# Optimization experiments

Measured on AMD Instinct MI355X. Metric: run time of the kernel, lower is better.

Reference implementation:

```python
import jax, jax.numpy as jnp
import numpy as np
import math

H = 16
D_ATTN = 64
D_MID = 64
D_X = 1024
D_Z = 1024
D_OUT = 1024
B = 2
L_X = 2048
L_Z = 2048
MINUS_INFINITY = -1000000.0

def _xavier(key, shape):
    fan_in, fan_out = shape
    limit = math.sqrt(6.0 / (fan_in + fan_out))
    return jax.random.uniform(key, shape, jnp.float32, -limit, limit)

def setup_inputs() -> dict:
    key = jax.random.key(0)
    ks = jax.random.split(key, 8)
    primary = jax.random.normal(ks[0], (B, L_X, D_X), jnp.float32)
    context = jax.random.normal(ks[1], (B, L_Z, D_Z), jnp.float32)
    padding_mask = jnp.ones((B, L_Z), jnp.int32)
    # causal attention mask (b, l_x, l_z)
    attention_mask = jnp.broadcast_to(
        jnp.tril(jnp.ones((L_X, L_Z), jnp.int32))[None], (B, L_X, L_Z))
    W_qs = _xavier(ks[2], (D_X, H * D_ATTN))
    W_ks = _xavier(ks[3], (D_Z, H * D_ATTN))
    W_vs = _xavier(ks[4], (D_Z, H * D_MID))
    W_o = _xavier(ks[5], (H * D_MID, D_OUT))
    b_o = jnp.zeros((D_OUT,), jnp.float32)
    return {"primary": primary, "context": context,
            "padding_mask": padding_mask, "attention_mask": attention_mask,
            "W_qs": W_qs, "W_ks": W_ks, "W_vs": W_vs, "W_o": W_o, "b_o": b_o}

def reference(primary, context, padding_mask, attention_mask, W_qs, W_ks, W_vs, W_o, b_o):
    b, l_x, _ = primary.shape
    l_z = context.shape[1]
    # QKV projections, split into heads (head-major columns)
    q = (primary @ W_qs).reshape(b, l_x, H, D_ATTN).transpose(0, 2, 1, 3)  # (b,h,l_x,d_attn)
    k = (context @ W_ks).reshape(b, l_z, H, D_ATTN).transpose(0, 2, 1, 3)  # (b,h,l_z,d_attn)
    v = (context @ W_vs).reshape(b, l_z, H, D_MID).transpose(0, 2, 1, 3)   # (b,h,l_z,d_mid)
    scores = jnp.einsum('bhxd,bhzd->bhxz', q, k) / math.sqrt(D_ATTN)
    # combined mask: attention_mask AND padding_mask, broadcast over heads
    mask = (attention_mask * padding_mask[:, None, :])[:, None]  # (b,1,l_x,l_z)
    scores = jnp.where(mask == 0, MINUS_INFINITY, scores)
    attn = jax.nn.softmax(scores, axis=-1)
    out = jnp.einsum('bhxz,bhzm->bhxm', attn, v)  # (b,h,l_x,d_mid)
    out = out.transpose(0, 2, 1, 3).reshape(b, l_x, H * D_MID)
    return out @ W_o + b_o
```

## Files before the change

kernel.cpp:

```cpp
#include <hip/hip_runtime.h>

#define NB 2
#define LX 2048
#define LZ 2048
#define HH 16
#define DA 64
#define DM 64
#define HD 1024
#define KVS 2048
#define MINF  -1000000.0f
#define QSC   0.1803368801f
#define DTHR  8.0f

typedef __attribute__((ext_vector_type(8))) short short8;
typedef __attribute__((ext_vector_type(4))) float f32x4;

static __device__ __forceinline__ ushort f2bf(float f) {
    union { float f; uint32_t u; } c; c.f = f;
    return (ushort)((c.u + 0x7FFFu + ((c.u >> 16) & 1u)) >> 16);
}

static __device__ __forceinline__ float bf2f(ushort u) {
    union { uint32_t u; float f; } c; c.u = (uint32_t)u << 16;
    return c.f;
}

static __device__ __forceinline__ uint32_t cvtpk(float lo, float hi) {
    uint32_t r;
    asm("v_cvt_pk_bf16_f32 %0, %1, %2" : "=v"(r) : "v"(lo), "v"(hi));
    return r;
}

#define GL16(g, l) __builtin_amdgcn_global_load_lds( \
    (const __attribute__((address_space(1))) void*)(g), \
    (__attribute__((address_space(3))) void*)(l), 16, 0, 0)

__global__ __launch_bounds__(256) void prep(
    const float* __restrict__ pA, const float* __restrict__ pB,
    ushort* __restrict__ oA, ushort* __restrict__ oB,
    const float* __restrict__ W0, const float* __restrict__ W1,
    const float* __restrict__ W2, const float* __restrict__ W3,
    ushort* __restrict__ T0, ushort* __restrict__ T1,
    ushort* __restrict__ T2, ushort* __restrict__ T3,
    const int* __restrict__ amask, const int* __restrict__ pmask,
    int* __restrict__ cls)
{
    const int fid = blockIdx.x;
    const int t = threadIdx.x;
    if (fid < 8192) {
        const int i = fid * 256 + t;
        const float* in = (i < 1048576) ? pA : pB;
        ushort* out = (i < 1048576) ? oA : oB;
        const int j = i & 1048575;
        float4 v = ((const float4*)in)[j];
        ushort4 o;
        o.x = f2bf(v.x); o.y = f2bf(v.y); o.z = f2bf(v.z); o.w = f2bf(v.w);
        ((ushort4*)out)[j] = o;
    } else if (fid < 9216) {
        __shared__ ushort Ls[64][72];
        const int id2 = fid - 8192;
        const int zz = id2 >> 8, rem = id2 & 255;
        const float* W = (zz == 0) ? W0 : (zz == 1) ? W1 : (zz == 2) ? W2 : W3;
        ushort* Wt = (zz == 0) ? T0 : (zz == 1) ? T1 : (zz == 2) ? T2 : T3;
        const int n0 = (rem & 15) * 64, k0 = (rem >> 4) * 64;
        const int rr = t >> 4, c4 = (t & 15) * 4;
        #pragma unroll
        for (int i = 0; i < 4; ++i) {
            const int r = rr + i * 16;
            float4 v = *(const float4*)&W[(size_t)(k0 + r) * 1024 + n0 + c4];
            Ls[c4 + 0][r] = f2bf(v.x);
            Ls[c4 + 1][r] = f2bf(v.y);
            Ls[c4 + 2][r] = f2bf(v.z);
            Ls[c4 + 3][r] = f2bf(v.w);
        }
        __syncthreads();
        const int n = t >> 2, kc = (t & 3) * 16;
        *(short8*)&Wt[(size_t)(n0 + n) * 1024 + k0 + kc]     = *(const short8*)&Ls[n][kc];
        *(short8*)&Wt[(size_t)(n0 + n) * 1024 + k0 + kc + 8] = *(const short8*)&Ls[n][kc + 8];
    } else {
        const int bid = fid - 9216;
        const int b = bid >> 10, xb = (bid >> 5) & 31, zb = bid & 31;
        int andv = 1, orv = 0;
        #pragma unroll
        for (int i = 0; i < 16; ++i) {
            const int e = t + i * 256;
            const int r = e >> 6, z = e & 63;
            const int m = amask[((size_t)b * LX + xb * 64 + r) * LZ + zb * 64 + z];
            const int p = pmask[(size_t)b * LZ + zb * 64 + z];
            const int v = (m != 0) & (p != 0);
            andv &= v; orv |= v;
        }
        __shared__ int sa[256];
        __shared__ int so[256];
        sa[t] = andv; so[t] = orv;
        __syncthreads();
        for (int s = 128; s > 0; s >>= 1) {
            if (t < s) { sa[t] &= sa[t + s]; so[t] |= so[t + s]; }
            __syncthreads();
        }
        if (t == 0) cls[bid] = so[0] ? (sa[0] ? 1 : 2) : 0;
    }
}

__global__ __launch_bounds__(256) void gemm_qkv(
    const ushort* __restrict__ Pb, const ushort* __restrict__ Cb,
    const ushort* __restrict__ Wqt, const ushort* __restrict__ Wkvt,
    ushort* __restrict__ Qb, ushort* __restrict__ KV)
{
    const int bx = blockIdx.x;
    const bool isQ = bx < 8;
    const ushort* A  = isQ ? Pb : Cb;
    const ushort* Bt = isQ ? Wqt : Wkvt;
    ushort* Cout = isQ ? Qb : KV;
    const int n0 = (isQ ? bx : bx - 8) * 128;
    const int ostr = isQ ? 1024 : KVS;
    const float osc = isQ ? QSC : 1.0f;

    __shared__ ushort As[128 * 32];
    __shared__ ushort Bs[128 * 32];
    const int t = threadIdx.x;
    const int w = t >> 6, l = t & 63, lr = l & 15, lg = l >> 4;
    const int wr = w >> 1, wc = w & 1;
    const int m0 = blockIdx.y * 128;

    const int c0 = t, c1 = t + 256;
    const ushort* a0 = &A[(size_t)(m0 + (c0 >> 2)) * 1024 + (c0 & 3) * 8];
    const ushort* a1 = &A[(size_t)(m0 + (c1 >> 2)) * 1024 + (c1 & 3) * 8];
    const ushort* b0 = &Bt[(size_t)(n0 + (c0 >> 2)) * 1024 + (c0 & 3) * 8];
    const ushort* b1 = &Bt[(size_t)(n0 + (c1 >> 2)) * 1024 + (c1 & 3) * 8];
    ushort* lA0 = &As[w * 512];
    ushort* lA1 = &As[(4 + w) * 512];
    ushort* lB0 = &Bs[w * 512];
    ushort* lB1 = &Bs[(4 + w) * 512];

    f32x4 acc[4][4];
    #pragma unroll
    for (int i = 0; i < 4; ++i)
        #pragma unroll
        for (int j = 0; j < 4; ++j) acc[i][j] = 0.f;

    for (int k0 = 0; k0 < 1024; k0 += 32) {
        __syncthreads();
        GL16(a0 + k0, lA0);
        GL16(a1 + k0, lA1);
        GL16(b0 + k0, lB0);
        GL16(b1 + k0, lB1);
        __syncthreads();
        short8 af[4], bf[4];
        #pragma unroll
        for (int mi = 0; mi < 4; ++mi)
            af[mi] = *(const short8*)&As[(wr * 64 + mi * 16 + lr) * 32 + lg * 8];
        #pragma unroll
        for (int nj = 0; nj < 4; ++nj)
            bf[nj] = *(const short8*)&Bs[(wc * 64 + nj * 16 + lr) * 32 + lg * 8];
        #pragma unroll
        for (int mi = 0; mi < 4; ++mi)
            #pragma unroll
            for (int nj = 0; nj < 4; ++nj)
                acc[mi][nj] = __builtin_amdgcn_mfma_f32_16x16x32_bf16(
                    af[mi], bf[nj], acc[mi][nj], 0, 0, 0);
    }

    const int row0 = m0 + wr * 64, col0 = n0 + wc * 64;
    #pragma unroll
    for (int mi = 0; mi < 4; ++mi)
        #pragma unroll
        for (int nj = 0; nj < 4; ++nj) {
            const int col = col0 + nj * 16 + lr;
            #pragma unroll
            for (int r = 0; r < 4; ++r) {
                const int row = row0 + mi * 16 + lg * 4 + r;
                Cout[(size_t)row * ostr + col] = f2bf(acc[mi][nj][r] * osc);
            }
        }
}

__global__ __launch_bounds__(256, 4) void attn_mfma(
    const ushort* __restrict__ Qg, const ushort* __restrict__ KVg,
    const int* __restrict__ amask, const int* __restrict__ pmask,
    const int* __restrict__ cls, ushort* __restrict__ Op,
    float2* __restrict__ ml)
{
    __shared__ ushort Ks[64 * 72];
    __shared__ ushort Vt[64 * 64];

    const int t = threadIdx.x, w = t >> 6, l = t & 63, lr = l & 15, lg = l >> 4;
    const int flat = blockIdx.x + 32 * (blockIdx.y + 16 * blockIdx.z);
    const int xcd = flat & 7, ii = flat >> 3;
    const int g = xcd + 8 * (ii >> 5);
    const int xr_ = ii & 31;
    const int h = g & 15, bs = g >> 4;
    const int b = bs & 1, sKV = bs >> 1;
    const int fx = (xr_ & 1) ? 31 - (xr_ >> 1) : (xr_ >> 1);
    const int qb = b ? 31 - fx : fx;
    const int qw = qb * 64 + w * 16;

    short8 qf[2];
    #pragma unroll
    for (int ks = 0; ks < 2; ++ks)
        qf[ks] = *(const short8*)&Qg[(size_t)(b * LX + qw + lr) * HD
                                     + h * DA + ks * 32 + lg * 8];

    float mrun = -1e30f, lrun = 0.f;
    f32x4 o[4];
    #pragma unroll
    for (int mj = 0; mj < 4; ++mj) o[mj] = 0.f;

    const int kz = t >> 2, kc = (t & 3) * 16;
    const int vz = (t >> 3) * 2, vc = (t & 7) * 8;

    for (int zb = sKV; zb < LZ / 64; zb += 2) {
        const int cl = cls[b * 1024 + qb * 32 + zb];
        if (cl == 0) continue;
        const int z0 = zb * 64;

        __syncthreads();
        {
            const ushort* kp = &KVg[(size_t)(b * LZ + z0 + kz) * KVS + h * DA + kc];
            *(short8*)&Ks[kz * 72 + kc]     = *(const short8*)kp;
            *(short8*)&Ks[kz * 72 + kc + 8] = *(const short8*)(kp + 8);
            const ushort* vp = &KVg[(size_t)(b * LZ + z0 + vz) * KVS + 1024 + h * DM + vc];
            short8 v0 = *(const short8*)vp;
            short8 v1 = *(const short8*)(vp + KVS);
            const int zc = vz >> 3, zo = vz & 7;
            #pragma unroll
            for (int j = 0; j < 8; ++j) {
                const int m = vc + j;
                const int idx = m * 64 + (((zc ^ m ^ (m >> 3)) & 7) << 3) + zo;
                *(uint32_t*)&Vt[idx] =
                    (uint32_t)(ushort)v0[j] | ((uint32_t)(ushort)v1[j] << 16);
            }
        }
        __syncthreads();

        f32x4 s[4];
        __builtin_amdgcn_s_setprio(1);
        #pragma unroll
        for (int nj = 0; nj < 4; ++nj) {
            const short8 kf0 = *(const short8*)&Ks[(nj * 16 + lr) * 72 + lg * 8];
            const short8 kf1 = *(const short8*)&Ks[(nj * 16 + lr) * 72 + 32 + lg * 8];
            f32x4 z4 = 0.f;
            z4 = __builtin_amdgcn_mfma_f32_16x16x32_bf16(kf0, qf[0], z4, 0, 0, 0);
            z4 = __builtin_amdgcn_mfma_f32_16x16x32_bf16(kf1, qf[1], z4, 0, 0, 0);
            s[nj] = z4;
        }
        __builtin_amdgcn_s_setprio(0);
        if (cl == 2) {
            const size_t arow = (size_t)(b * LX + qw + lr) * LZ + z0;
            #pragma unroll
            for (int nj = 0; nj < 4; ++nj)
                #pragma unroll
                for (int r = 0; r < 4; ++r) {
                    const int z = nj * 16 + lg * 4 + r;
                    const int ok = (amask[arow + z] != 0) & (pmask[b * LZ + z0 + z] != 0);
                    if (!ok) s[nj][r] = MINF;
                }
        }
        {
            float pm = s[0][0];
            #pragma unroll
            for (int nj = 0; nj < 4; ++nj)
                #pragma unroll
                for (int r = 0; r < 4; ++r) pm = fmaxf(pm, s[nj][r]);
            pm = fmaxf(pm, __shfl_xor(pm, 16));
            pm = fmaxf(pm, __shfl_xor(pm, 32));
            if (__any(pm > mrun + DTHR)) {
                const float mn = fmaxf(mrun, pm);
                const float al = exp2f(mrun - mn);
                mrun = mn;
                lrun *= al;
                #pragma unroll
                for (int r = 0; r < 4; ++r) {
                    const float alq = __shfl(al, (lg << 2) + r);
                    #pragma unroll
                    for (int mj = 0; mj < 4; ++mj) o[mj][r] *= alq;
                }
            }
            #pragma unroll
            for (int nj = 0; nj < 4; ++nj)
                #pragma unroll
                for (int r = 0; r < 4; ++r) {
                    const float p = exp2f(s[nj][r] - mrun);
                    s[nj][r] = p;
                    lrun += p;
                }
        }
        short8 pa[2];
        {
            uint32_t pk01[4], pk23[4];
            #pragma unroll
            for (int nj = 0; nj < 4; ++nj) {
                pk01[nj] = cvtpk(s[nj][0], s[nj][1]);
                pk23[nj] = cvtpk(s[nj][2], s[nj][3]);
            }
            #pragma unroll
            for (int ks = 0; ks < 2; ++ks) {
                union { uint32_t d[4]; short8 v; } u;
                u.d[0] = pk01[2 * ks];
                u.d[1] = pk23[2 * ks];
                u.d[2] = pk01[2 * ks + 1];
                u.d[3] = pk23[2 * ks + 1];
                pa[ks] = u.v;
            }
        }
        __builtin_amdgcn_s_setprio(1);
        #pragma unroll
        for (int mj = 0; mj < 4; ++mj) {
            const int m_ = mj * 16 + lr;
            const int xr = (m_ ^ (m_ >> 3)) & 7;
            const int czb = lg >> 1;
            const int zo = (lg & 1) * 4;
            #pragma unroll
            for (int ks = 0; ks < 2; ++ks) {
                const int clo = (ks * 4 + czb) ^ xr;
                const int chi = (ks * 4 + 2 + czb) ^ xr;
                const uint2 lo = *(const uint2*)&Vt[m_ * 64 + ((clo & 7) << 3) + zo];
                const uint2 hi = *(const uint2*)&Vt[m_ * 64 + ((chi & 7) << 3) + zo];
                union { uint32_t d[4]; short8 v; } u;
                u.d[0] = lo.x; u.d[1] = lo.y; u.d[2] = hi.x; u.d[3] = hi.y;
                o[mj] = __builtin_amdgcn_mfma_f32_16x16x32_bf16(pa[ks], u.v, o[mj], 0, 0, 0);
            }
        }
        __builtin_amdgcn_s_setprio(0);
    }

    lrun += __shfl_xor(lrun, 16);
    lrun += __shfl_xor(lrun, 32);
    if (l < 16)
        ml[(size_t)((sKV * NB + b) * HH + h) * LX + qw + l] = make_float2(mrun, lrun);
    const size_t ob = (size_t)((sKV * NB + b) * LX + qw) * HD + h * DM;
    #pragma unroll
    for (int r = 0; r < 4; ++r)
        #pragma unroll
        for (int mj = 0; mj < 4; ++mj)
            Op[ob + (size_t)((lg << 2) + r) * HD + mj * 16 + lr] = f2bf(o[mj][r]);
}

__global__ __launch_bounds__(256) void gemm_out_fused(
    const ushort* __restrict__ Op, const float2* __restrict__ ml,
    const ushort* __restrict__ Bt, const float* __restrict__ bias,
    float* __restrict__ Cout)
{
    __shared__ ushort As[64 * 32];
    __shared__ ushort Bs[128 * 32];
    __shared__ float2 Wl[64][17];
    const int t = threadIdx.x;
    const int w = t >> 6, l = t & 63, lr = l & 15, lg = l >> 4;
    const int wr = w >> 1, wc = w & 1;
    const int n0 = blockIdx.x * 128, m0 = blockIdx.y * 64;

    {
        const int e = t * 4;
        #pragma unroll
        for (int j = 0; j < 4; ++j) {
            const int rl = (e + j) >> 4, hh = (e + j) & 15;
            const int ra = m0 + rl;
            const int bb = ra >> 11, xx = ra & 2047;
            const float2 a0 = ml[(size_t)(bb * HH + hh) * LX + xx];
            const float2 a1 = ml[(size_t)((NB + bb) * HH + hh) * LX + xx];
            const float M = fmaxf(a0.x, a1.x);
            const float w0 = exp2f(a0.x - M), w1 = exp2f(a1.x - M);
            const float inv = 1.f / fmaxf(a0.y * w0 + a1.y * w1, 1e-37f);
            Wl[rl][hh] = make_float2(w0 * inv, w1 * inv);
        }
    }
    __syncthreads();

    const int ra = m0 + (t >> 2), ka = (t & 3) * 8;
    const ushort* p0 = &Op[(size_t)ra * HD + ka];
    const ushort* p1 = p0 + (size_t)NB * LX * HD;
    const ushort* b0 = &Bt[(size_t)(n0 + (t >> 2)) * 1024 + ka];
    const ushort* b1 = &Bt[(size_t)(n0 + 64 + (t >> 2)) * 1024 + ka];
    ushort* lB0 = &Bs[w * 512];
    ushort* lB1 = &Bs[(4 + w) * 512];

    f32x4 acc[2][4];
    #pragma unroll
    for (int i = 0; i < 2; ++i)
        #pragma unroll
        for (int j = 0; j < 4; ++j) acc[i][j] = 0.f;

    for (int k0 = 0; k0 < 1024; k0 += 32) {
        const short8 q0 = *(const short8*)(p0 + k0);
        const short8 q1 = *(const short8*)(p1 + k0);
        const float2 wv = Wl[t >> 2][(k0 + ka) >> 6];
        union { ushort d[8]; short8 v; } av;
        #pragma unroll
        for (int j = 0; j < 8; ++j)
            av.d[j] = f2bf(bf2f((ushort)q0[j]) * wv.x + bf2f((ushort)q1[j]) * wv.y);
        __syncthreads();
        *(short8*)&As[t * 8] = av.v;
        GL16(b0 + k0, lB0);
        GL16(b1 + k0, lB1);
        __syncthreads();
        short8 af[2], bf[4];
        #pragma unroll
        for (int mi = 0; mi < 2; ++mi)
            af[mi] = *(const short8*)&As[(wr * 32 + mi * 16 + lr) * 32 + lg * 8];
        #pragma unroll
        for (int nj = 0; nj < 4; ++nj)
            bf[nj] = *(const short8*)&Bs[(wc * 64 + nj * 16 + lr) * 32 + lg * 8];
        #pragma unroll
        for (int mi = 0; mi < 2; ++mi)
            #pragma unroll
            for (int nj = 0; nj < 4; ++nj)
                acc[mi][nj] = __builtin_amdgcn_mfma_f32_16x16x32_bf16(
                    af[mi], bf[nj], acc[mi][nj], 0, 0, 0);
    }

    const int row0 = m0 + wr * 32, col0 = n0 + wc * 64;
    #pragma unroll
    for (int mi = 0; mi < 2; ++mi)
        #pragma unroll
        for (int nj = 0; nj < 4; ++nj) {
            const int col = col0 + nj * 16 + lr;
            #pragma unroll
            for (int r = 0; r < 4; ++r) {
                const int row = row0 + mi * 16 + lg * 4 + r;
                Cout[(size_t)row * 1024 + col] = acc[mi][nj][r] + bias[col];
            }
        }
}

extern "C" void kernel_launch(void* const* d_in, const int* in_sizes, int n_in,
                              void* d_out, int out_size, void* d_ws, size_t ws_size,
                              hipStream_t stream)
{
    const float* primary = (const float*)d_in[0];
    const float* context = (const float*)d_in[1];
    const int*   pmask   = (const int*)d_in[2];
    const int*   amask   = (const int*)d_in[3];
    const float* Wq      = (const float*)d_in[4];
    const float* Wk      = (const float*)d_in[5];
    const float* Wv      = (const float*)d_in[6];
    const float* Wo      = (const float*)d_in[7];
    const float* bo      = (const float*)d_in[8];
    float* out = (float*)d_out;

    char* w8 = (char*)d_ws;
    ushort* Pb  = (ushort*)(w8 + 0);
    ushort* Cb  = (ushort*)(w8 + 8388608);
    ushort* Qb  = (ushort*)(w8 + 16777216);
    ushort* KV  = (ushort*)(w8 + 25165824);
    ushort* Wqt = (ushort*)(w8 + 50331648);
    ushort* Wkt = (ushort*)(w8 + 52428800);
    ushort* Wvt = (ushort*)(w8 + 54525952);
    ushort* Wot = (ushort*)(w8 + 56623104);
    int*    clsp = (int*)(w8 + 58720256);
    ushort* Op   = Pb;
    float2* mlp  = (float2*)Wqt;

    prep<<<11264, 256, 0, stream>>>(primary, context, Pb, Cb,
                                    Wq, Wk, Wv, Wo, Wqt, Wkt, Wvt, Wot,
                                    amask, pmask, clsp);
    gemm_qkv<<<dim3(24, 32), 256, 0, stream>>>(Pb, Cb, Wqt, Wkt, Qb, KV);
    attn_mfma<<<dim3(32, 16, 4), 256, 0, stream>>>(Qb, KV, amask, pmask, clsp, Op, mlp);
    gemm_out_fused<<<dim3(8, 64), 256, 0, stream>>>(Op, mlp, Wot, bo, out);
}
```

Baseline: 134.9 us.

## Rewrite QKV GEMM with 256x256 tiles and triple-buffered async LDS pipeline

Replaces the 128x128 QKV projection GEMM with a 512-thread kernel computing 256x256 tiles. It uses a three-stage LDS ring buffer, so global-to-LDS loads for stage k+2 are issued while MFMAs run on stage k. It synchronises with vmcnt waits plus a single barrier per step and raises wave priority around the MFMA block. The larger tiles raise arithmetic intensity but cut the grid to 192 blocks, which may underfill the GPU, and the 96KB of LDS limits occupancy.

```diff
diff --git a/kernel.cpp b/kernel.cpp
--- a/kernel.cpp
+++ b/kernel.cpp
@@ -102,68 +102,103 @@
     }
 }
 
-__global__ __launch_bounds__(256) void gemm_qkv(
+__global__ __launch_bounds__(512, 2) void gemm_qkv256(
     const ushort* __restrict__ Pb, const ushort* __restrict__ Cb,
     const ushort* __restrict__ Wqt, const ushort* __restrict__ Wkvt,
     ushort* __restrict__ Qb, ushort* __restrict__ KV)
 {
-    const int bx = blockIdx.x;
-    const bool isQ = bx < 8;
+    __shared__ ushort lds[49152];
+
+    const int bid = blockIdx.x;
+    const bool isQ = bid < 64;
     const ushort* A  = isQ ? Pb : Cb;
     const ushort* Bt = isQ ? Wqt : Wkvt;
     ushort* Cout = isQ ? Qb : KV;
-    const int n0 = (isQ ? bx : bx - 8) * 128;
     const int ostr = isQ ? 1024 : KVS;
     const float osc = isQ ? QSC : 1.0f;
-
-    __shared__ ushort As[128 * 32];
-    __shared__ ushort Bs[128 * 32];
+    int mt, nt;
+    if (isQ) { mt = bid >> 2; nt = bid & 3; }
+    else     { const int i2 = bid - 64; mt = i2 >> 3; nt = i2 & 7; }
+    const int m0 = mt * 256, n0 = nt * 256;
+
     const int t = threadIdx.x;
     const int w = t >> 6, l = t & 63, lr = l & 15, lg = l >> 4;
-    const int wr = w >> 1, wc = w & 1;
-    const int m0 = blockIdx.y * 128;
-
-    const int c0 = t, c1 = t + 256;
-    const ushort* a0 = &A[(size_t)(m0 + (c0 >> 2)) * 1024 + (c0 & 3) * 8];
-    const ushort* a1 = &A[(size_t)(m0 + (c1 >> 2)) * 1024 + (c1 & 3) * 8];
-    const ushort* b0 = &Bt[(size_t)(n0 + (c0 >> 2)) * 1024 + (c0 & 3) * 8];
-    const ushort* b1 = &Bt[(size_t)(n0 + (c1 >> 2)) * 1024 + (c1 & 3) * 8];
-    ushort* lA0 = &As[w * 512];
-    ushort* lA1 = &As[(4 + w) * 512];
-    ushort* lB0 = &Bs[w * 512];
-    ushort* lB1 = &Bs[(4 + w) * 512];
-
-    f32x4 acc[4][4];
-    #pragma unroll
-    for (int i = 0; i < 4; ++i)
-        #pragma unroll
-        for (int j = 0; j < 4; ++j) acc[i][j] = 0.f;
-
-    for (int k0 = 0; k0 < 1024; k0 += 32) {
-        __syncthreads();
-        GL16(a0 + k0, lA0);
-        GL16(a1 + k0, lA1);
-        GL16(b0 + k0, lB0);
-        GL16(b1 + k0, lB1);
-        __syncthreads();
-        short8 af[4], bf[4];
-        #pragma unroll
-        for (int mi = 0; mi < 4; ++mi)
-            af[mi] = *(const short8*)&As[(wr * 64 + mi * 16 + lr) * 32 + lg * 8];
+    const int wm = w >> 2, wn = w & 3;
+
+    const int rA0 = t >> 2, cA0 = (t & 3) * 8;
+    const int rA1 = (t + 512) >> 2, cA1 = ((t + 512) & 3) * 8;
+    const ushort* srcA0 = &A[(size_t)(m0 + rA0) * 1024 + cA0];
+    const ushort* srcA1 = &A[(size_t)(m0 + rA1) * 1024 + cA1];
+    const ushort* srcB0 = &Bt[(size_t)(n0 + rA0) * 1024 + cA0];
+    const ushort* srcB1 = &Bt[(size_t)(n0 + rA1) * 1024 + cA1];
+    const int dA0 = (w * 64) * 8;
+    const int dA1 = (w * 64 + 512) * 8;
+
+    int aoff[8], boff[4];
+    #pragma unroll
+    for (int mi = 0; mi < 8; ++mi) {
+        const int row = wm * 128 + mi * 16 + lr;
+        aoff[mi] = row * 32 + lg * 8;
+    }
+    #pragma unroll
+    for (int nj = 0; nj < 4; ++nj) {
+        const int row = wn * 64 + nj * 16 + lr;
+        boff[nj] = 8192 + row * 32 + lg * 8;
+    }
+
+#define QSTAGE(kk, bufbase) do {                                   \
+        const int k0s = (kk) * 32;                                 \
+        GL16(srcA0 + k0s, &lds[(bufbase) + dA0]);                  \
+        GL16(srcA1 + k0s, &lds[(bufbase) + dA1]);                  \
+        GL16(srcB0 + k0s, &lds[(bufbase) + 8192 + dA0]);           \
+        GL16(srcB1 + k0s, &lds[(bufbase) + 8192 + dA1]);           \
+    } while (0)
+
+    f32x4 acc[8][4];
+    #pragma unroll
+    for (int mi = 0; mi < 8; ++mi)
+        #pragma unroll
+        for (int nj = 0; nj < 4; ++nj) acc[mi][nj] = 0.f;
+
+    int bcur = 0, bnxt = 16384, bnx2 = 32768;
+
+    QSTAGE(0, bcur);
+    QSTAGE(1, bnxt);
+    asm volatile("s_waitcnt vmcnt(4)" ::: "memory");
+    __builtin_amdgcn_s_barrier();
+    __builtin_amdgcn_sched_barrier(0);
+
+    for (int j = 0; j < 32; ++j) {
+        QSTAGE((j + 2) & 31, bnx2);
+
+        short8 af[8], bf[4];
+        #pragma unroll
+        for (int mi = 0; mi < 8; ++mi)
+            af[mi] = *(const short8*)&lds[bcur + aoff[mi]];
         #pragma unroll
         for (int nj = 0; nj < 4; ++nj)
-            bf[nj] = *(const short8*)&Bs[(wc * 64 + nj * 16 + lr) * 32 + lg * 8];
-        #pragma unroll
-        for (int mi = 0; mi < 4; ++mi)
+            bf[nj] = *(const short8*)&lds[bcur + boff[nj]];
+
+        __builtin_amdgcn_s_setprio(1);
+        #pragma unroll
+        for (int mi = 0; mi < 8; ++mi)
             #pragma unroll
             for (int nj = 0; nj < 4; ++nj)
                 acc[mi][nj] = __builtin_amdgcn_mfma_f32_16x16x32_bf16(
                     af[mi], bf[nj], acc[mi][nj], 0, 0, 0);
-    }
-
-    const int row0 = m0 + wr * 64, col0 = n0 + wc * 64;
-    #pragma unroll
-    for (int mi = 0; mi < 4; ++mi)
+        __builtin_amdgcn_s_setprio(0);
+
+        asm volatile("s_waitcnt vmcnt(4)" ::: "memory");
+        __builtin_amdgcn_s_barrier();
+        __builtin_amdgcn_sched_barrier(0);
+
+        const int tmp = bcur; bcur = bnxt; bnxt = bnx2; bnx2 = tmp;
+    }
+#undef QSTAGE
+
+    const int row0 = m0 + wm * 128, col0 = n0 + wn * 64;
+    #pragma unroll
+    for (int mi = 0; mi < 8; ++mi)
         #pragma unroll
         for (int nj = 0; nj < 4; ++nj) {
             const int col = col0 + nj * 16 + lr;
@@ -453,7 +488,7 @@
     prep<<<11264, 256, 0, stream>>>(primary, context, Pb, Cb,
                                     Wq, Wk, Wv, Wo, Wqt, Wkt, Wvt, Wot,
                                     amask, pmask, clsp);
-    gemm_qkv<<<dim3(24, 32), 256, 0, stream>>>(Pb, Cb, Wqt, Wkt, Qb, KV);
+    gemm_qkv256<<<192, 512, 0, stream>>>(Pb, Cb, Wqt, Wkt, Qb, KV);
     attn_mfma<<<dim3(32, 16, 4), 256, 0, stream>>>(Qb, KV, amask, pmask, clsp, Op, mlp);
     gemm_out_fused<<<dim3(8, 64), 256, 0, stream>>>(Op, mlp, Wot, bo, out);
 }
```

After: 135.4 us. About the same (+0.4%).

## Double-buffer K/V tiles in LDS with register prefetch and ballot-based block skipping

Applied to the files above, without the earlier changes.

The attention kernel now double-buffers the K and V^T tiles in shared memory. The next active key block's global loads are issued into registers before computing on the current block, so load latency overlaps the MFMA and softmax work, and only one barrier is needed per iteration. The per-block class lookups are replaced with two wave ballots that build bitmasks of active and mixed blocks, and workgroups with no active blocks write neutral outputs and exit early. This costs double the LDS and extra live registers, which may reduce occupancy under launch_bounds(256,4).

```diff
diff --git a/kernel.cpp b/kernel.cpp
--- a/kernel.cpp
+++ b/kernel.cpp
@@ -181,8 +181,8 @@
     const int* __restrict__ cls, ushort* __restrict__ Op,
     float2* __restrict__ ml)
 {
-    __shared__ ushort Ks[64 * 72];
-    __shared__ ushort Vt[64 * 64];
+    __shared__ ushort Ks[2][64 * 72];
+    __shared__ ushort Vt[2][64 * 64];
 
     const int t = threadIdx.x, w = t >> 6, l = t & 63, lr = l & 15, lg = l >> 4;
     const int flat = blockIdx.x + 32 * (blockIdx.y + 16 * blockIdx.z);
@@ -195,6 +195,24 @@
     const int qb = b ? 31 - fx : fx;
     const int qw = qb * 64 + w * 16;
 
+    const uint32_t halfm = sKV ? 0xAAAAAAAAu : 0x55555555u;
+    const int cv = cls[b * 1024 + qb * 32 + (l & 31)];
+    const uint32_t act = (uint32_t)__ballot(cv != 0) & halfm;
+    const uint32_t mix = (uint32_t)__ballot(cv == 2) & halfm;
+
+    const size_t obase = (size_t)((sKV * NB + b) * LX + qw) * HD + h * DM;
+    if (act == 0) {
+        if (l < 16)
+            ml[(size_t)((sKV * NB + b) * HH + h) * LX + qw + l]
+                = make_float2(-1e30f, 0.f);
+        #pragma unroll
+        for (int r = 0; r < 4; ++r)
+            #pragma unroll
+            for (int mj = 0; mj < 4; ++mj)
+                Op[obase + (size_t)((lg << 2) + r) * HD + mj * 16 + lr] = 0;
+        return;
+    }
+
     short8 qf[2];
     #pragma unroll
     for (int ks = 0; ks < 2; ++ks)
@@ -209,43 +227,61 @@
     const int kz = t >> 2, kc = (t & 3) * 16;
     const int vz = (t >> 3) * 2, vc = (t & 7) * 8;
 
-    for (int zb = sKV; zb < LZ / 64; zb += 2) {
-        const int cl = cls[b * 1024 + qb * 32 + zb];
-        if (cl == 0) continue;
+    short8 kr0, kr1, vr0, vr1;
+
+#define PREFETCH(zbx) do {                                                     \
+        const int z0p = (zbx) * 64;                                           \
+        const ushort* kp = &KVg[(size_t)(b * LZ + z0p + kz) * KVS + h * DA + kc];\
+        kr0 = *(const short8*)kp;                                             \
+        kr1 = *(const short8*)(kp + 8);                                       \
+        const ushort* vp = &KVg[(size_t)(b * LZ + z0p + vz) * KVS + 1024 + h * DM + vc];\
+        vr0 = *(const short8*)vp;                                             \
+        vr1 = *(const short8*)(vp + KVS);                                     \
+    } while (0)
+
+#define WRITE_LDS(bi) do {                                                     \
+        *(short8*)&Ks[bi][kz * 72 + kc]     = kr0;                            \
+        *(short8*)&Ks[bi][kz * 72 + kc + 8] = kr1;                            \
+        const int zc = vz >> 3, zo = vz & 7;                                  \
+        _Pragma("unroll")                                                      \
+        for (int j = 0; j < 8; ++j) {                                         \
+            const int m = vc + j;                                             \
+            const int idx = m * 64 + (((zc ^ m ^ (m >> 3)) & 7) << 3) + zo;   \
+            *(uint32_t*)&Vt[bi][idx] =                                        \
+                (uint32_t)(ushort)vr0[j] | ((uint32_t)(ushort)vr1[j] << 16);  \
+        }                                                                      \
+    } while (0)
+
+    int zb = __builtin_ctz(act);
+    uint32_t rem = act & (act - 1);
+    PREFETCH(zb);
+    WRITE_LDS(0);
+    __syncthreads();
+    int cur = 0;
+
+    for (;;) {
+        const bool mixed = (mix >> zb) & 1;
         const int z0 = zb * 64;
-
-        __syncthreads();
-        {
-            const ushort* kp = &KVg[(size_t)(b * LZ + z0 + kz) * KVS + h * DA + kc];
-            *(short8*)&Ks[kz * 72 + kc]     = *(const short8*)kp;
-            *(short8*)&Ks[kz * 72 + kc + 8] = *(const short8*)(kp + 8);
-            const ushort* vp = &KVg[(size_t)(b * LZ + z0 + vz) * KVS + 1024 + h * DM + vc];
-            short8 v0 = *(const short8*)vp;
-            short8 v1 = *(const short8*)(vp + KVS);
-            const int zc = vz >> 3, zo = vz & 7;
-            #pragma unroll
-            for (int j = 0; j < 8; ++j) {
-                const int m = vc + j;
-                const int idx = m * 64 + (((zc ^ m ^ (m >> 3)) & 7) << 3) + zo;
-                *(uint32_t*)&Vt[idx] =
-                    (uint32_t)(ushort)v0[j] | ((uint32_t)(ushort)v1[j] << 16);
-            }
-        }
-        __syncthreads();
+        int zbn = -1;
+        if (rem) {
+            zbn = __builtin_ctz(rem);
+            rem &= rem - 1;
+            PREFETCH(zbn);
+        }
 
         f32x4 s[4];
         __builtin_amdgcn_s_setprio(1);
         #pragma unroll
         for (int nj = 0; nj < 4; ++nj) {
-            const short8 kf0 = *(const short8*)&Ks[(nj * 16 + lr) * 72 + lg * 8];
-            const short8 kf1 = *(const short8*)&Ks[(nj * 16 + lr) * 72 + 32 + lg * 8];
+            const short8 kf0 = *(const short8*)&Ks[cur][(nj * 16 + lr) * 72 + lg * 8];
+            const short8 kf1 = *(const short8*)&Ks[cur][(nj * 16 + lr) * 72 + 32 + lg * 8];
             f32x4 z4 = 0.f;
             z4 = __builtin_amdgcn_mfma_f32_16x16x32_bf16(kf0, qf[0], z4, 0, 0, 0);
             z4 = __builtin_amdgcn_mfma_f32_16x16x32_bf16(kf1, qf[1], z4, 0, 0, 0);
             s[nj] = z4;
         }
         __builtin_amdgcn_s_setprio(0);
-        if (cl == 2) {
+        if (mixed) {
             const size_t arow = (size_t)(b * LX + qw + lr) * LZ + z0;
             #pragma unroll
             for (int nj = 0; nj < 4; ++nj)
@@ -314,26 +350,33 @@
             for (int ks = 0; ks < 2; ++ks) {
                 const int clo = (ks * 4 + czb) ^ xr;
                 const int chi = (ks * 4 + 2 + czb) ^ xr;
-                const uint2 lo = *(const uint2*)&Vt[m_ * 64 + ((clo & 7) << 3) + zo];
-                const uint2 hi = *(const uint2*)&Vt[m_ * 64 + ((chi & 7) << 3) + zo];
+                const uint2 lo = *(const uint2*)&Vt[cur][m_ * 64 + ((clo & 7) << 3) + zo];
+                const uint2 hi = *(const uint2*)&Vt[cur][m_ * 64 + ((chi & 7) << 3) + zo];
                 union { uint32_t d[4]; short8 v; } u;
                 u.d[0] = lo.x; u.d[1] = lo.y; u.d[2] = hi.x; u.d[3] = hi.y;
                 o[mj] = __builtin_amdgcn_mfma_f32_16x16x32_bf16(pa[ks], u.v, o[mj], 0, 0, 0);
             }
         }
         __builtin_amdgcn_s_setprio(0);
+
+        if (zbn < 0) break;
+        WRITE_LDS(cur ^ 1);
+        __syncthreads();
+        cur ^= 1;
+        zb = zbn;
     }
 
     lrun += __shfl_xor(lrun, 16);
     lrun += __shfl_xor(lrun, 32);
     if (l < 16)
         ml[(size_t)((sKV * NB + b) * HH + h) * LX + qw + l] = make_float2(mrun, lrun);
-    const size_t ob = (size_t)((sKV * NB + b) * LX + qw) * HD + h * DM;
     #pragma unroll
     for (int r = 0; r < 4; ++r)
         #pragma unroll
         for (int mj = 0; mj < 4; ++mj)
-            Op[ob + (size_t)((lg << 2) + r) * HD + mj * 16 + lr] = f2bf(o[mj][r]);
+            Op[obase + (size_t)((lg << 2) + r) * HD + mj * 16 + lr] = f2bf(o[mj][r]);
+#undef PREFETCH
+#undef WRITE_LDS
 }
 
 __global__ __launch_bounds__(256) void gemm_out_fused(
```

New measurement: 137.4 us. No clear change (+1.9%).

## Write V transposed from QKV GEMM and load V fragments directly in attention

Applied to the files above, without the earlier changes.

The QKV GEMM now writes K into its own buffer and V transposed (head-dim major), staging the transpose through shared memory. The attention kernel drops its per-tile LDS V transpose. It loads K with swizzled direct global-to-LDS copies and reads V fragments straight from global memory into registers. Blocks whose KV tiles are all masked now exit early and write zeros. This removes LDS scatter work and one barrier per tile, at the cost of extra epilogue work in the GEMM and uncached global V reads that may add latency.

```diff
diff --git a/kernel.cpp b/kernel.cpp
--- a/kernel.cpp
+++ b/kernel.cpp
@@ -7,7 +7,6 @@
 #define DA 64
 #define DM 64
 #define HD 1024
-#define KVS 2048
 #define MINF  -1000000.0f
 #define QSC   0.1803368801f
 #define DTHR  8.0f
@@ -105,19 +104,20 @@
 __global__ __launch_bounds__(256) void gemm_qkv(
     const ushort* __restrict__ Pb, const ushort* __restrict__ Cb,
     const ushort* __restrict__ Wqt, const ushort* __restrict__ Wkvt,
-    ushort* __restrict__ Qb, ushort* __restrict__ KV)
+    ushort* __restrict__ Qb, ushort* __restrict__ Kb, ushort* __restrict__ VT)
 {
+    __shared__ ushort sh[8704];
+    ushort* As = sh;
+    ushort* Bs = sh + 4096;
+
     const int bx = blockIdx.x;
     const bool isQ = bx < 8;
+    const bool isV = bx >= 16;
     const ushort* A  = isQ ? Pb : Cb;
     const ushort* Bt = isQ ? Wqt : Wkvt;
-    ushort* Cout = isQ ? Qb : KV;
     const int n0 = (isQ ? bx : bx - 8) * 128;
-    const int ostr = isQ ? 1024 : KVS;
     const float osc = isQ ? QSC : 1.0f;
 
-    __shared__ ushort As[128 * 32];
-    __shared__ ushort Bs[128 * 32];
     const int t = threadIdx.x;
     const int w = t >> 6, l = t & 63, lr = l & 15, lg = l >> 4;
     const int wr = w >> 1, wc = w & 1;
@@ -161,28 +161,54 @@
                     af[mi], bf[nj], acc[mi][nj], 0, 0, 0);
     }
 
-    const int row0 = m0 + wr * 64, col0 = n0 + wc * 64;
-    #pragma unroll
-    for (int mi = 0; mi < 4; ++mi)
-        #pragma unroll
-        for (int nj = 0; nj < 4; ++nj) {
-            const int col = col0 + nj * 16 + lr;
-            #pragma unroll
-            for (int r = 0; r < 4; ++r) {
-                const int row = row0 + mi * 16 + lg * 4 + r;
-                Cout[(size_t)row * ostr + col] = f2bf(acc[mi][nj][r] * osc);
-            }
-        }
+    if (!isV) {
+        ushort* Cout = isQ ? Qb : Kb;
+        const int row0 = m0 + wr * 64, col0 = n0 + wc * 64;
+        #pragma unroll
+        for (int mi = 0; mi < 4; ++mi)
+            #pragma unroll
+            for (int nj = 0; nj < 4; ++nj) {
+                const int col = col0 + nj * 16 + lr;
+                #pragma unroll
+                for (int r = 0; r < 4; ++r) {
+                    const int row = row0 + mi * 16 + lg * 4 + r;
+                    Cout[(size_t)row * 1024 + col] = f2bf(acc[mi][nj][r] * osc);
+                }
+            }
+    } else {
+        #pragma unroll
+        for (int h2 = 0; h2 < 2; ++h2) {
+            __syncthreads();
+            if (wc == h2) {
+                #pragma unroll
+                for (int nj = 0; nj < 4; ++nj)
+                    #pragma unroll
+                    for (int mi = 0; mi < 4; ++mi)
+                        #pragma unroll
+                        for (int r = 0; r < 4; ++r)
+                            sh[(nj * 16 + lr) * 136 + wr * 64 + mi * 16 + lg * 4 + r]
+                                = f2bf(acc[mi][nj][r]);
+            }
+            __syncthreads();
+            const int vcl = t >> 2, seg = t & 3;
+            const int vcol = (n0 - 1024) + h2 * 64 + vcl;
+            ushort* dst = &VT[(size_t)vcol * 4096 + m0 + seg * 32];
+            const ushort* srcl = &sh[vcl * 136 + seg * 32];
+            *(short8*)(dst + 0)  = *(const short8*)(srcl + 0);
+            *(short8*)(dst + 8)  = *(const short8*)(srcl + 8);
+            *(short8*)(dst + 16) = *(const short8*)(srcl + 16);
+            *(short8*)(dst + 24) = *(const short8*)(srcl + 24);
+        }
+    }
 }
 
 __global__ __launch_bounds__(256, 4) void attn_mfma(
-    const ushort* __restrict__ Qg, const ushort* __restrict__ KVg,
-    const int* __restrict__ amask, const int* __restrict__ pmask,
-    const int* __restrict__ cls, ushort* __restrict__ Op,
-    float2* __restrict__ ml)
+    const ushort* __restrict__ Qg, const ushort* __restrict__ Kb,
+    const ushort* __restrict__ VT, const int* __restrict__ amask,
+    const int* __restrict__ pmask, const int* __restrict__ cls,
+    ushort* __restrict__ Op, float2* __restrict__ ml)
 {
-    __shared__ ushort Ks[64 * 72];
-    __shared__ ushort Vt[64 * 64];
+    __shared__ ushort Ks[64 * 64];
 
     const int t = threadIdx.x, w = t >> 6, l = t & 63, lr = l & 15, lg = l >> 4;
     const int flat = blockIdx.x + 32 * (blockIdx.y + 16 * blockIdx.z);
@@ -195,6 +221,24 @@
     const int qb = b ? 31 - fx : fx;
     const int qw = qb * 64 + w * 16;
 
+    const uint32_t halfm = sKV ? 0xAAAAAAAAu : 0x55555555u;
+    const int cv = cls[b * 1024 + qb * 32 + (l & 31)];
+    const uint32_t act = (uint32_t)__ballot(cv != 0) & halfm;
+    const uint32_t mix = (uint32_t)__ballot(cv == 2) & halfm;
+
+    const size_t obase = (size_t)((sKV * NB + b) * LX + qw) * HD + h * DM;
+    if (act == 0) {
+        if (l < 16)
+            ml[(size_t)((sKV * NB + b) * HH + h) * LX + qw + l]
+                = make_float2(-1e30f, 0.f);
+        #pragma unroll
+        for (int r = 0; r < 4; ++r)
+            #pragma unroll
+            for (int mj = 0; mj < 4; ++mj)
+                Op[obase + (size_t)((lg << 2) + r) * HD + mj * 16 + lr] = 0;
+        return;
+    }
+
     short8 qf[2];
     #pragma unroll
     for (int ks = 0; ks < 2; ++ks)
@@ -206,8 +250,12 @@
     #pragma unroll
     for (int mj = 0; mj < 4; ++mj) o[mj] = 0.f;
 
-    const int kz = t >> 2, kc = (t & 3) * 16;
-    const int vz = (t >> 3) * 2, vc = (t & 7) * 8;
+    const int zs0 = t >> 3, zs1 = 32 + (t >> 3);
+    const int cs = t & 7;
+    const int gc0 = (cs ^ (zs0 & 7)) << 3;
+    ushort* dst0 = &Ks[w * 512];
+    ushort* dst1 = &Ks[2048 + w * 512];
+    const size_t kbase = (size_t)(b * LZ) * 1024 + h * DA;
 
     for (int zb = sKV; zb < LZ / 64; zb += 2) {
         const int cl = cls[b * 1024 + qb * 32 + zb];
@@ -215,30 +263,29 @@
         const int z0 = zb * 64;
 
         __syncthreads();
-        {
-            const ushort* kp = &KVg[(size_t)(b * LZ + z0 + kz) * KVS + h * DA + kc];
-            *(short8*)&Ks[kz * 72 + kc]     = *(const short8*)kp;
-            *(short8*)&Ks[kz * 72 + kc + 8] = *(const short8*)(kp + 8);
-            const ushort* vp = &KVg[(size_t)(b * LZ + z0 + vz) * KVS + 1024 + h * DM + vc];
-            short8 v0 = *(const short8*)vp;
-            short8 v1 = *(const short8*)(vp + KVS);
-            const int zc = vz >> 3, zo = vz & 7;
-            #pragma unroll
-            for (int j = 0; j < 8; ++j) {
-                const int m = vc + j;
-                const int idx = m * 64 + (((zc ^ m ^ (m >> 3)) & 7) << 3) + zo;
-                *(uint32_t*)&Vt[idx] =
-                    (uint32_t)(ushort)v0[j] | ((uint32_t)(ushort)v1[j] << 16);
-            }
-        }
-        __syncthreads();
+        GL16(&Kb[kbase + (size_t)(z0 + zs0) * 1024 + gc0], dst0);
+        GL16(&Kb[kbase + (size_t)(z0 + zs1) * 1024 + gc0], dst1);
+        __syncthreads();
+
+        uint2 vlo[4][2], vhi[4][2];
+        #pragma unroll
+        for (int mj = 0; mj < 4; ++mj)
+            #pragma unroll
+            for (int ks = 0; ks < 2; ++ks) {
+                const ushort* vb = &VT[(size_t)(h * 64 + mj * 16 + lr) * 4096
+                                       + b * LZ + z0 + ks * 32 + lg * 4];
+                vlo[mj][ks] = *(const uint2*)vb;
+                vhi[mj][ks] = *(const uint2*)(vb + 16);
+            }
 
         f32x4 s[4];
         __builtin_amdgcn_s_setprio(1);
         #pragma unroll
         for (int nj = 0; nj < 4; ++nj) {
-            const short8 kf0 = *(const short8*)&Ks[(nj * 16 + lr) * 72 + lg * 8];
-            const short8 kf1 = *(const short8*)&Ks[(nj * 16 + lr) * 72 + 32 + lg * 8];
+            const int row = nj * 16 + lr;
+            const int sw = row & 7;
+            const short8 kf0 = *(const short8*)&Ks[row * 64 + ((lg ^ sw) << 3)];
+            const short8 kf1 = *(const short8*)&Ks[row * 64 + (((4 + lg) ^ sw) << 3)];
             f32x4 z4 = 0.f;
             z4 = __builtin_amdgcn_mfma_f32_16x16x32_bf16(kf0, qf[0], z4, 0, 0, 0);
             z4 = __builtin_amdgcn_mfma_f32_16x16x32_bf16(kf1, qf[1], z4, 0, 0, 0);
@@ -305,22 +352,14 @@
         }
         __builtin_amdgcn_s_setprio(1);
         #pragma unroll
-        for (int mj = 0; mj < 4; ++mj) {
-            const int m_ = mj * 16 + lr;
-            const int xr = (m_ ^ (m_ >> 3)) & 7;
-            const int czb = lg >> 1;
-            const int zo = (lg & 1) * 4;
+        for (int mj = 0; mj < 4; ++mj)
             #pragma unroll
             for (int ks = 0; ks < 2; ++ks) {
-                const int clo = (ks * 4 + czb) ^ xr;
-                const int chi = (ks * 4 + 2 + czb) ^ xr;
-                const uint2 lo = *(const uint2*)&Vt[m_ * 64 + ((clo & 7) << 3) + zo];
-                const uint2 hi = *(const uint2*)&Vt[m_ * 64 + ((chi & 7) << 3) + zo];
                 union { uint32_t d[4]; short8 v; } u;
-                u.d[0] = lo.x; u.d[1] = lo.y; u.d[2] = hi.x; u.d[3] = hi.y;
+                u.d[0] = vlo[mj][ks].x; u.d[1] = vlo[mj][ks].y;
+                u.d[2] = vhi[mj][ks].x; u.d[3] = vhi[mj][ks].y;
                 o[mj] = __builtin_amdgcn_mfma_f32_16x16x32_bf16(pa[ks], u.v, o[mj], 0, 0, 0);
             }
-        }
         __builtin_amdgcn_s_setprio(0);
     }
 
@@ -328,12 +367,11 @@
     lrun += __shfl_xor(lrun, 32);
     if (l < 16)
         ml[(size_t)((sKV * NB + b) * HH + h) * LX + qw + l] = make_float2(mrun, lrun);
-    const size_t ob = (size_t)((sKV * NB + b) * LX + qw) * HD + h * DM;
     #pragma unroll
     for (int r = 0; r < 4; ++r)
         #pragma unroll
         for (int mj = 0; mj < 4; ++mj)
-            Op[ob + (size_t)((lg << 2) + r) * HD + mj * 16 + lr] = f2bf(o[mj][r]);
+            Op[obase + (size_t)((lg << 2) + r) * HD + mj * 16 + lr] = f2bf(o[mj][r]);
 }
 
 __global__ __launch_bounds__(256) void gemm_out_fused(
@@ -441,7 +479,8 @@
     ushort* Pb  = (ushort*)(w8 + 0);
     ushort* Cb  = (ushort*)(w8 + 8388608);
     ushort* Qb  = (ushort*)(w8 + 16777216);
-    ushort* KV  = (ushort*)(w8 + 25165824);
+    ushort* Kb  = (ushort*)(w8 + 25165824);
+    ushort* VT  = (ushort*)(w8 + 33554432);
     ushort* Wqt = (ushort*)(w8 + 50331648);
     ushort* Wkt = (ushort*)(w8 + 52428800);
     ushort* Wvt = (ushort*)(w8 + 54525952);
@@ -453,7 +492,7 @@
     prep<<<11264, 256, 0, stream>>>(primary, context, Pb, Cb,
                                     Wq, Wk, Wv, Wo, Wqt, Wkt, Wvt, Wot,
                                     amask, pmask, clsp);
-    gemm_qkv<<<dim3(24, 32), 256, 0, stream>>>(Pb, Cb, Wqt, Wkt, Qb, KV);
-    attn_mfma<<<dim3(32, 16, 4), 256, 0, stream>>>(Qb, KV, amask, pmask, clsp, Op, mlp);
+    gemm_qkv<<<dim3(24, 32), 256, 0, stream>>>(Pb, Cb, Wqt, Wkt, Qb, Kb, VT);
+    attn_mfma<<<dim3(32, 16, 4), 256, 0, stream>>>(Qb, Kb, VT, amask, pmask, clsp, Op, mlp);
     gemm_out_fused<<<dim3(8, 64), 256, 0, stream>>>(Op, mlp, Wot, bo, out);
 }
```

Result: slower. 265.3 us (+96.7%).
